# Performance work log

Measured on AMD Instinct MI355X. Metric: run time of the kernel, lower is better.

The kernel has to match this reference:

```python
import jax, jax.numpy as jnp
import numpy as np

D_MODEL = 2048
NUM_HEAD = 16
HEAD_DIM = D_MODEL // NUM_HEAD


def setup_inputs() -> dict:
    key = jax.random.key(0)
    ks = jax.random.split(key, 5)
    scale = 1.0 / np.sqrt(D_MODEL)
    x = jax.random.normal(ks[0], (2, 2048, D_MODEL), dtype=jnp.float32)
    wq = jax.random.normal(ks[1], (D_MODEL, D_MODEL), dtype=jnp.float32) * scale
    wk = jax.random.normal(ks[2], (D_MODEL, D_MODEL), dtype=jnp.float32) * scale
    wv = jax.random.normal(ks[3], (D_MODEL, D_MODEL), dtype=jnp.float32) * scale
    wo = jax.random.normal(ks[4], (D_MODEL, D_MODEL), dtype=jnp.float32) * scale
    return {"x": x, "wq": wq, "wk": wk, "wv": wv, "wo": wo}


def _split_heads(t):
    # [B, T, D] -> [B, H, T, dk]
    B, T, _ = t.shape
    return t.reshape(B, T, NUM_HEAD, HEAD_DIM).transpose(0, 2, 1, 3)


def reference(x, wq, wk, wv, wo):
    # nn.Linear computes x @ W.T; weights here are [out, in]
    Q = _split_heads(x @ wq.T)
    K = _split_heads(x @ wk.T)
    V = _split_heads(x @ wv.T)
    scale = 1.0 / jnp.sqrt(jnp.asarray(HEAD_DIM, dtype=x.dtype))
    score = jnp.einsum('bhqd,bhkd->bhqk', Q, K) * scale
    Tq = score.shape[-2]
    causal_mask = jnp.triu(jnp.ones((Tq, Tq), dtype=bool), k=1)
    score = jnp.where(causal_mask, -jnp.inf, score)
    attn = jax.nn.softmax(score, axis=-1)
    out = jnp.einsum('bhqk,bhkd->bhqd', attn, V)
    B, H, T, dk = out.shape
    out = out.transpose(0, 2, 1, 3).reshape(B, T, H * dk)
    return out @ wo.T
```

## Files before the change

kernel.cpp:

```cpp
#include <hip/hip_runtime.h>

#define DM    2048
#define NH    16
#define HD    128
#define TSEQ  2048
#define BATCH 2
#define MROWS (BATCH * TSEQ)

typedef __bf16 bf16_t;
typedef __bf16 bf16x8 __attribute__((ext_vector_type(8)));
typedef __bf16 bf16x4 __attribute__((ext_vector_type(4)));
typedef float  f32x4  __attribute__((ext_vector_type(4)));
typedef float  f32x16 __attribute__((ext_vector_type(16)));
typedef unsigned short u16x8 __attribute__((ext_vector_type(8)));
typedef unsigned int   u32;

static __device__ __forceinline__ unsigned short f2bf_bits(float f) {
  unsigned u = __builtin_bit_cast(unsigned, f);
  u += 0x7fffu + ((u >> 16) & 1u);
  return (unsigned short)(u >> 16);
}
static __device__ __forceinline__ bf16_t f2bf(float f) {
  unsigned short h = f2bf_bits(f);
  return __builtin_bit_cast(bf16_t, h);
}

static __device__ __forceinline__ void gll16(const void* g, void* lds) {
  __builtin_amdgcn_global_load_lds(
      (const __attribute__((address_space(1))) unsigned int*)g,
      (__attribute__((address_space(3))) unsigned int*)lds, 16, 0, 0);
}

static __device__ __forceinline__ float fast_exp2(float x) {
#if __has_builtin(__builtin_amdgcn_exp2f)
  return __builtin_amdgcn_exp2f(x);
#else
  return exp2f(x);
#endif
}
static __device__ __forceinline__ float fast_rcp(float x) {
#if __has_builtin(__builtin_amdgcn_rcpf)
  return __builtin_amdgcn_rcpf(x);
#else
  return 1.0f / x;
#endif
}

static __device__ __forceinline__ u32 cvtpk(float a, float b) {
  u32 d;
  asm("v_cvt_pk_bf16_f32 %0, %1, %2" : "=v"(d) : "v"(a), "v"(b));
  return d;
}
static __device__ __forceinline__ void pl32swap(u32& a, u32& b) {
  asm volatile("v_permlane32_swap_b32 %0, %1" : "+v"(a), "+v"(b));
}

__global__ void cvt_bf16(const float* __restrict__ s, bf16_t* __restrict__ d, int n8) {
  int i = blockIdx.x * blockDim.x + threadIdx.x;
  if (i >= n8) return;
  const float4* sp = reinterpret_cast<const float4*>(s);
  float4 a = sp[2 * i], b = sp[2 * i + 1];
  u16x8 o;
  o[0] = f2bf_bits(a.x); o[1] = f2bf_bits(a.y); o[2] = f2bf_bits(a.z); o[3] = f2bf_bits(a.w);
  o[4] = f2bf_bits(b.x); o[5] = f2bf_bits(b.y); o[6] = f2bf_bits(b.z); o[7] = f2bf_bits(b.w);
  reinterpret_cast<u16x8*>(d)[i] = o;
}

__global__ void cvt_bf16_w4(const float* __restrict__ s0, const float* __restrict__ s1,
                            const float* __restrict__ s2, const float* __restrict__ s3,
                            bf16_t* __restrict__ d, int n8seg) {
  int i = blockIdx.x * blockDim.x + threadIdx.x;
  if (i >= n8seg) return;
  const int seg = blockIdx.y;
  const float* s = (seg == 0) ? s0 : (seg == 1) ? s1 : (seg == 2) ? s2 : s3;
  const float4* sp = reinterpret_cast<const float4*>(s);
  float4 a = sp[2 * i], b = sp[2 * i + 1];
  u16x8 o;
  o[0] = f2bf_bits(a.x); o[1] = f2bf_bits(a.y); o[2] = f2bf_bits(a.z); o[3] = f2bf_bits(a.w);
  o[4] = f2bf_bits(b.x); o[5] = f2bf_bits(b.y); o[6] = f2bf_bits(b.z); o[7] = f2bf_bits(b.w);
  reinterpret_cast<u16x8*>(d + (size_t)seg * DM * DM)[i] = o;
}

template <int OUTM>
__global__ __launch_bounds__(512, 1) void gemm_3buf(
    const bf16_t* __restrict__ A, const bf16_t* __restrict__ B,
    void* __restrict__ Cq, void* __restrict__ Ck, void* __restrict__ Cv) {
  __shared__ bf16_t Asm[3][256 * 64];
  __shared__ bf16_t Bsm[3][128 * 64];
  const int tid = threadIdx.x;
  const int l = tid & 63, w = tid >> 6;
  const int wm = w >> 1, wn = w & 1;
  const int m0 = blockIdx.y * 256, n0 = blockIdx.x * 128;
  const int NT = DM / 64;

  auto SA = [&](int t, int buf, int s) {
    const int rowbase = s * 64 + w * 8;
    const int row = rowbase + (l >> 3);
    const int ug = (l & 7) ^ (row & 7);
    const int tc = (t < NT) ? t : 0;
    gll16(A + (size_t)(m0 + row) * DM + tc * 64 + ug * 8,
          (char*)Asm[buf] + rowbase * 128);
  };
  auto SB = [&](int t, int buf, int s) {
    const int rowbase = s * 64 + w * 8;
    const int row = rowbase + (l >> 3);
    const int ug = (l & 7) ^ (row & 7);
    const int tc = (t < NT) ? t : 0;
    gll16(B + (size_t)(n0 + row) * DM + tc * 64 + ug * 8,
          (char*)Bsm[buf] + rowbase * 128);
  };

  f32x4 acc[4][4] = {};

#pragma unroll
  for (int s = 0; s < 4; ++s) SA(0, 0, s);
  SB(0, 0, 0); SB(0, 0, 1);
#pragma unroll
  for (int s = 0; s < 4; ++s) SA(1, 1, s);
  SB(1, 1, 0); SB(1, 1, 1);
  asm volatile("s_waitcnt vmcnt(6)" ::: "memory");
  __builtin_amdgcn_s_barrier();
  __builtin_amdgcn_sched_barrier(0);

  for (int j = 0; j < NT; ++j) {
    const int bj = j % 3, bs = (j + 2) % 3;
    const char* Ab_ = (const char*)Asm[bj];
    const char* Bb_ = (const char*)Bsm[bj];
    bf16x8 af[4][2], bfr[4][2];

#pragma unroll
    for (int mi = 0; mi < 4; ++mi)
#pragma unroll
      for (int kh = 0; kh < 2; ++kh) {
        const int row = wm * 64 + mi * 16 + (l & 15);
        const int u = (kh * 4 + (l >> 4)) ^ (row & 7);
        af[mi][kh] = *reinterpret_cast<const bf16x8*>(Ab_ + row * 128 + u * 16);
      }
#pragma unroll
    for (int ni = 0; ni < 4; ++ni)
#pragma unroll
      for (int kh = 0; kh < 2; ++kh) {
        const int row = wn * 64 + ni * 16 + (l & 15);
        const int u = (kh * 4 + (l >> 4)) ^ (row & 7);
        bfr[ni][kh] = *reinterpret_cast<const bf16x8*>(Bb_ + row * 128 + u * 16);
      }

    SA(j + 2, bs, 0); SA(j + 2, bs, 1); SA(j + 2, bs, 2); SA(j + 2, bs, 3);
    SB(j + 2, bs, 0); SB(j + 2, bs, 1);
    __builtin_amdgcn_sched_barrier(0);

    __builtin_amdgcn_s_setprio(1);
#pragma unroll
    for (int kh = 0; kh < 2; ++kh)
#pragma unroll
      for (int mi = 0; mi < 4; ++mi)
#pragma unroll
        for (int ni = 0; ni < 4; ++ni)
          acc[mi][ni] = __builtin_amdgcn_mfma_f32_16x16x32_bf16(
              af[mi][kh], bfr[ni][kh], acc[mi][ni], 0, 0, 0);
    __builtin_amdgcn_s_setprio(0);

    asm volatile("s_waitcnt vmcnt(6)" ::: "memory");
    __builtin_amdgcn_s_barrier();
    __builtin_amdgcn_sched_barrier(0);
  }

  if constexpr (OUTM == 0) {
    const int proj = n0 >> 11;
    const int nc0 = n0 & (DM - 1);
    if (proj < 2) {
      bf16_t* C = (bf16_t*)(proj == 0 ? Cq : Ck);
#pragma unroll
      for (int mi = 0; mi < 4; ++mi) {
        const int row = m0 + wm * 64 + mi * 16 + ((l >> 4) << 2);
#pragma unroll
        for (int ni = 0; ni < 4; ++ni) {
          const int col = nc0 + wn * 64 + ni * 16 + (l & 15);
#pragma unroll
          for (int r = 0; r < 4; ++r)
            C[(size_t)(row + r) * DM + col] = f2bf(acc[mi][ni][r]);
        }
      }
    } else {
      bf16_t* VT = (bf16_t*)Cv;
#pragma unroll
      for (int mi = 0; mi < 4; ++mi) {
        const int row = m0 + wm * 64 + mi * 16 + ((l >> 4) << 2);
        const int bb = row >> 11, tt = row & (TSEQ - 1);
#pragma unroll
        for (int ni = 0; ni < 4; ++ni) {
          const int col = nc0 + wn * 64 + ni * 16 + (l & 15);
          const int hh = col >> 7, dd = col & (HD - 1);
          bf16x4 pk;
#pragma unroll
          for (int r = 0; r < 4; ++r) pk[r] = f2bf(acc[mi][ni][r]);
          *reinterpret_cast<bf16x4*>(VT + (((size_t)bb * NH + hh) * HD + dd) * TSEQ + tt) = pk;
        }
      }
    }
  } else {
    float* C = (float*)Cq;
#pragma unroll
    for (int mi = 0; mi < 4; ++mi) {
      const int row = m0 + wm * 64 + mi * 16 + ((l >> 4) << 2);
#pragma unroll
      for (int ni = 0; ni < 4; ++ni) {
        const int col = n0 + wn * 64 + ni * 16 + (l & 15);
#pragma unroll
        for (int r = 0; r < 4; ++r)
          C[(size_t)(row + r) * DM + col] = acc[mi][ni][r];
      }
    }
  }
}

#define LDS_TOT 75776
__global__ __launch_bounds__(512, 2) void flash_attn(
    const bf16_t* __restrict__ Q, const bf16_t* __restrict__ Kx,
    const bf16_t* __restrict__ VT, bf16_t* __restrict__ O) {
  __shared__ __align__(16) char Lds[LDS_TOT];

  const int tid = threadIdx.x;
  const int l = tid & 63, w = tid >> 6;
  const int hi = l >> 5, ln31 = l & 31;
  const int qw = w >> 1, kw = w & 1;
  const int bh = blockIdx.y;
  const int b = bh >> 4, h = bh & 15;
  const size_t base   = ((size_t)b * TSEQ) * DM + (size_t)h * HD;
  const size_t vtbase = ((size_t)b * NH + h) * HD * (size_t)TSEQ;
  const float cc = 0.12752775f;

  auto run_qtile = [&](int qb) {
    const int wq0 = qb * 128 + qw * 32;
    const int nt = 2 * qb + 2;

    bf16x8 qf[8];
    {
      const bf16_t* qp = Q + base + (size_t)(wq0 + ln31) * DM + hi * 8;
#pragma unroll
      for (int m = 0; m < 8; ++m)
        qf[m] = *reinterpret_cast<const bf16x8*>(qp + m * 16);
    }

    f32x16 acc[4] = {};
    float mrow = -1e30f, lrow = 0.f;

    auto STAGE = [&](int t, int buf) {
#pragma unroll
      for (int c = 0; c < 2; ++c) {
        const int chunk = w * 2 + c;
        const int krow = chunk * 4 + (l >> 4);
        const int u = l & 15;
        const int ug = (u & 8) | ((u ^ krow) & 7);
        gll16(Kx + base + (size_t)(t * 64 + krow) * DM + ug * 8,
              Lds + buf * 16384 + chunk * 1024);
      }
#pragma unroll
      for (int c = 0; c < 2; ++c) {
        const int ci = w * 2 + c;
        const int d = ci * 8 + (l >> 3);
        const int ug = (l & 7) ^ (l >> 3);
        gll16(VT + vtbase + (size_t)d * TSEQ + t * 64 + ug * 8,
              Lds + 32768 + buf * 16384 + ci * 1024);
      }
    };

    STAGE(0, 0);
    __syncthreads();
    int cur = 0;

    for (int t = 0; t < nt; ++t) {
      if (t + 1 < nt) STAGE(t + 1, cur ^ 1);

      const bool active = (t * 64 + kw * 32 <= wq0 + 31);
      if (active) {
        f32x16 s = {};
        const char* Kb_ = Lds + cur * 16384;
        const int kvr = kw * 32 + ln31;
#pragma unroll
        for (int m = 0; m < 8; ++m) {
          const int u = 2 * m + hi;
          const int uswz = (u & 8) | ((u ^ kvr) & 7);
          const bf16x8 kf = *reinterpret_cast<const bf16x8*>(Kb_ + kvr * 256 + uswz * 16);
          s = __builtin_amdgcn_mfma_f32_32x32x16_bf16(kf, qf[m], s, 0, 0, 0);
        }

        float sv[16];
        const int qg = wq0 + ln31;
#pragma unroll
        for (int r = 0; r < 16; ++r) sv[r] = s[r] * cc;
        if (t * 64 + kw * 32 + 31 > wq0) {
#pragma unroll
          for (int r = 0; r < 16; ++r) {
            const int kvg = t * 64 + kw * 32 + (r & 3) + 8 * (r >> 2) + 4 * hi;
            if (kvg > qg) sv[r] = -3.0e38f;
          }
        }

        float mt = sv[0];
#pragma unroll
        for (int r = 1; r < 16; ++r) mt = fmaxf(mt, sv[r]);
        mt = fmaxf(mt, __shfl_xor(mt, 32, 64));

        if (__any(mt > mrow + 8.0f)) {
          const float mn = fmaxf(mrow, mt);
          const float scl = fast_exp2(mrow - mn);
          mrow = mn;
          lrow *= scl;
#pragma unroll
          for (int r = 0; r < 16; ++r) {
            const float sr = __shfl(scl, (r & 3) + 8 * (r >> 2) + 4 * hi, 64);
            acc[0][r] *= sr; acc[1][r] *= sr; acc[2][r] *= sr; acc[3][r] *= sr;
          }
        }

        float rs = 0.f;
#pragma unroll
        for (int r = 0; r < 16; ++r) {
          const float p = fast_exp2(sv[r] - mrow);
          sv[r] = p;
          rs += p;
        }
        rs += __shfl_xor(rs, 32, 64);
        lrow += rs;

        u32 frag[2][4];
#pragma unroll
        for (int f = 0; f < 2; ++f) {
          const float* p = &sv[f * 8];
          u32 a1 = cvtpk(p[0], p[1]);
          u32 b1 = cvtpk(p[4], p[5]);
          pl32swap(a1, b1);
          u32 a2 = cvtpk(p[2], p[3]);
          u32 b2 = cvtpk(p[6], p[7]);
          pl32swap(a2, b2);
          frag[f][0] = a1; frag[f][1] = a2; frag[f][2] = b1; frag[f][3] = b2;
        }

        const char* Vb_ = Lds + 32768 + cur * 16384;
#pragma unroll
        for (int f = 0; f < 2; ++f) {
          const bf16x8 pf = __builtin_bit_cast(bf16x8, *reinterpret_cast<u32(*)[4]>(frag[f]));
#pragma unroll
          for (int n = 0; n < 4; ++n) {
            const int d = n * 32 + ln31;
            const int u = (kw * 2 + f) * 2 + hi;
            const int uswz = u ^ (d & 7);
            const bf16x8 vf = *reinterpret_cast<const bf16x8*>(Vb_ + d * 128 + uswz * 16);
            acc[n] = __builtin_amdgcn_mfma_f32_32x32x16_bf16(pf, vf, acc[n], 0, 0, 0);
          }
        }
      }
      __syncthreads();
      cur ^= 1;
    }

    {
      float* accb = (float*)(Lds + qw * 16384 + kw * 8192);
      const int nb = (kw == 0) ? 2 : 0;
#pragma unroll
      for (int np = 0; np < 2; ++np) {
        float* dst = accb + np * 1024;
#pragma unroll
        for (int r = 0; r < 16; ++r) {
          const int row = (r & 3) + 8 * (r >> 2) + 4 * hi;
          dst[row * 32 + ln31] = acc[nb + np][r];
        }
      }
      float* mlp = (float*)(Lds + 65536 + qw * 1024 + kw * 512);
      if (hi == 0) { mlp[ln31] = mrow; mlp[32 + ln31] = lrow; }
      __syncthreads();

      const float* mlo = (float*)(Lds + 65536 + qw * 1024 + (kw ^ 1) * 512);
      const float mo = mlo[ln31], lo = mlo[32 + ln31];
      const float mm = fmaxf(mrow, mo);
      const float as = fast_exp2(mrow - mm);
      const float ao = fast_exp2(mo - mm);
      const float rln = fast_rcp(lrow * as + lo * ao);
      float* ml2p = (float*)(Lds + 69632 + qw * 1536 + kw * 768);
      if (hi == 0) { ml2p[ln31] = as; ml2p[32 + ln31] = ao; ml2p[64 + ln31] = rln; }
      __syncthreads();

      const float* accoth = (float*)(Lds + qw * 16384 + (kw ^ 1) * 8192);
      const int nf = (kw == 0) ? 0 : 2;
#pragma unroll
      for (int r = 0; r < 16; ++r) {
        const int row = (r & 3) + 8 * (r >> 2) + 4 * hi;
        const float asr = ml2p[row];
        const float aor = ml2p[32 + row];
        const float rlr = ml2p[64 + row];
        const int q = wq0 + row;
        bf16_t* op = O + base + (size_t)q * DM + ln31;
#pragma unroll
        for (int np = 0; np < 2; ++np) {
          const float vo = (acc[nf + np][r] * asr + accoth[np * 1024 + row * 32 + ln31] * aor) * rlr;
          op[(kw * 2 + np) * 32] = f2bf(vo);
        }
      }
      __syncthreads();
    }
  };

  const int i = blockIdx.x;
  run_qtile(i);
  run_qtile((int)(TSEQ / 128) - 1 - i);
}

extern "C" void kernel_launch(void* const* d_in, const int* in_sizes, int n_in,
                              void* d_out, int out_size, void* d_ws, size_t ws_size,
                              hipStream_t stream) {
  (void)in_sizes; (void)n_in; (void)out_size; (void)ws_size;
  const float* x  = (const float*)d_in[0];
  const float* wq = (const float*)d_in[1];
  const float* wk = (const float*)d_in[2];
  const float* wv = (const float*)d_in[3];
  const float* wo = (const float*)d_in[4];
  float* out = (float*)d_out;

  const size_t nx = (size_t)MROWS * DM;
  const size_t nw = (size_t)DM * DM;
  bf16_t* xb  = (bf16_t*)d_ws;
  bf16_t* wqb = xb + nx;
  bf16_t* Qb  = wqb + 4 * nw;
  bf16_t* Kb  = Qb + nx;
  bf16_t* Vtb = Kb + nx;
  bf16_t* Ab  = Vtb + nx;
  bf16_t* wob = wqb + 3 * nw;

  cvt_bf16<<<(int)(nx / 8 / 256), 256, 0, stream>>>(x, xb, (int)(nx / 8));
  cvt_bf16_w4<<<dim3((int)(nw / 8 / 256), 4), 256, 0, stream>>>(
      wq, wk, wv, wo, wqb, (int)(nw / 8));

  gemm_3buf<0><<<dim3(3 * DM / 128, MROWS / 256), 512, 0, stream>>>(
      xb, wqb, Qb, Kb, Vtb);

  flash_attn<<<dim3(TSEQ / 256, BATCH * NH), 512, 0, stream>>>(Qb, Kb, Vtb, Ab);

  gemm_3buf<1><<<dim3(DM / 128, MROWS / 256), 512, 0, stream>>>(
      Ab, wob, out, nullptr, nullptr);
}
```

Measured before the change: 224.1 us.

## Halve GEMM K-tile to 32 and allow two blocks per CU

The projection GEMM now uses a K-step of 32 instead of 64. This halves the triple-buffered LDS footprint, and the launch bounds are raised to allow two 512-thread blocks per CU. The LDS swizzle and load mapping are rewritten for 64-byte rows, and the wait counts are adjusted to match. The aim is more occupancy to hide memory latency, at the cost of twice as many barriers per K and fewer MFMAs between syncs, with tighter register limits.

```diff
diff --git a/kernel.cpp b/kernel.cpp
--- a/kernel.cpp
+++ b/kernel.cpp
@@ -82,43 +82,37 @@
 }
 
 template <int OUTM>
-__global__ __launch_bounds__(512, 1) void gemm_3buf(
+__global__ __launch_bounds__(512, 2) void gemm_3buf(
     const bf16_t* __restrict__ A, const bf16_t* __restrict__ B,
     void* __restrict__ Cq, void* __restrict__ Ck, void* __restrict__ Cv) {
-  __shared__ bf16_t Asm[3][256 * 64];
-  __shared__ bf16_t Bsm[3][128 * 64];
+  __shared__ bf16_t Asm[3][256 * 32];
+  __shared__ bf16_t Bsm[3][128 * 32];
   const int tid = threadIdx.x;
   const int l = tid & 63, w = tid >> 6;
   const int wm = w >> 1, wn = w & 1;
   const int m0 = blockIdx.y * 256, n0 = blockIdx.x * 128;
-  const int NT = DM / 64;
+  const int NT = DM / 32;
 
   auto SA = [&](int t, int buf, int s) {
-    const int rowbase = s * 64 + w * 8;
-    const int row = rowbase + (l >> 3);
-    const int ug = (l & 7) ^ (row & 7);
+    const int row = s * 128 + (tid >> 2);
+    const int ug = (tid & 3) ^ ((row >> 1) & 3);
     const int tc = (t < NT) ? t : 0;
-    gll16(A + (size_t)(m0 + row) * DM + tc * 64 + ug * 8,
-          (char*)Asm[buf] + rowbase * 128);
+    gll16(A + (size_t)(m0 + row) * DM + tc * 32 + ug * 8,
+          (char*)Asm[buf] + s * 8192 + tid * 16);
   };
-  auto SB = [&](int t, int buf, int s) {
-    const int rowbase = s * 64 + w * 8;
-    const int row = rowbase + (l >> 3);
-    const int ug = (l & 7) ^ (row & 7);
+  auto SB = [&](int t, int buf) {
+    const int row = tid >> 2;
+    const int ug = (tid & 3) ^ ((row >> 1) & 3);
     const int tc = (t < NT) ? t : 0;
-    gll16(B + (size_t)(n0 + row) * DM + tc * 64 + ug * 8,
-          (char*)Bsm[buf] + rowbase * 128);
+    gll16(B + (size_t)(n0 + row) * DM + tc * 32 + ug * 8,
+          (char*)Bsm[buf] + tid * 16);
   };
 
   f32x4 acc[4][4] = {};
 
-#pragma unroll
-  for (int s = 0; s < 4; ++s) SA(0, 0, s);
-  SB(0, 0, 0); SB(0, 0, 1);
-#pragma unroll
-  for (int s = 0; s < 4; ++s) SA(1, 1, s);
-  SB(1, 1, 0); SB(1, 1, 1);
-  asm volatile("s_waitcnt vmcnt(6)" ::: "memory");
+  SA(0, 0, 0); SA(0, 0, 1); SB(0, 0);
+  SA(1, 1, 0); SA(1, 1, 1); SB(1, 1);
+  asm volatile("s_waitcnt vmcnt(3)" ::: "memory");
   __builtin_amdgcn_s_barrier();
   __builtin_amdgcn_sched_barrier(0);
 
@@ -126,41 +120,34 @@
     const int bj = j % 3, bs = (j + 2) % 3;
     const char* Ab_ = (const char*)Asm[bj];
     const char* Bb_ = (const char*)Bsm[bj];
-    bf16x8 af[4][2], bfr[4][2];
-
+    bf16x8 af[4], bfr[4];
+
+#pragma unroll
+    for (int mi = 0; mi < 4; ++mi) {
+      const int row = wm * 64 + mi * 16 + (l & 15);
+      const int u = (l >> 4) ^ ((row >> 1) & 3);
+      af[mi] = *reinterpret_cast<const bf16x8*>(Ab_ + row * 64 + u * 16);
+    }
+#pragma unroll
+    for (int ni = 0; ni < 4; ++ni) {
+      const int row = wn * 64 + ni * 16 + (l & 15);
+      const int u = (l >> 4) ^ ((row >> 1) & 3);
+      bfr[ni] = *reinterpret_cast<const bf16x8*>(Bb_ + row * 64 + u * 16);
+    }
+
+    SA(j + 2, bs, 0); SA(j + 2, bs, 1); SB(j + 2, bs);
+    __builtin_amdgcn_sched_barrier(0);
+
+    __builtin_amdgcn_s_setprio(1);
 #pragma unroll
     for (int mi = 0; mi < 4; ++mi)
 #pragma unroll
-      for (int kh = 0; kh < 2; ++kh) {
-        const int row = wm * 64 + mi * 16 + (l & 15);
-        const int u = (kh * 4 + (l >> 4)) ^ (row & 7);
-        af[mi][kh] = *reinterpret_cast<const bf16x8*>(Ab_ + row * 128 + u * 16);
-      }
-#pragma unroll
-    for (int ni = 0; ni < 4; ++ni)
-#pragma unroll
-      for (int kh = 0; kh < 2; ++kh) {
-        const int row = wn * 64 + ni * 16 + (l & 15);
-        const int u = (kh * 4 + (l >> 4)) ^ (row & 7);
-        bfr[ni][kh] = *reinterpret_cast<const bf16x8*>(Bb_ + row * 128 + u * 16);
-      }
-
-    SA(j + 2, bs, 0); SA(j + 2, bs, 1); SA(j + 2, bs, 2); SA(j + 2, bs, 3);
-    SB(j + 2, bs, 0); SB(j + 2, bs, 1);
-    __builtin_amdgcn_sched_barrier(0);
-
-    __builtin_amdgcn_s_setprio(1);
-#pragma unroll
-    for (int kh = 0; kh < 2; ++kh)
-#pragma unroll
-      for (int mi = 0; mi < 4; ++mi)
-#pragma unroll
-        for (int ni = 0; ni < 4; ++ni)
-          acc[mi][ni] = __builtin_amdgcn_mfma_f32_16x16x32_bf16(
-              af[mi][kh], bfr[ni][kh], acc[mi][ni], 0, 0, 0);
+      for (int ni = 0; ni < 4; ++ni)
+        acc[mi][ni] = __builtin_amdgcn_mfma_f32_16x16x32_bf16(
+            af[mi], bfr[ni], acc[mi][ni], 0, 0, 0);
     __builtin_amdgcn_s_setprio(0);
 
-    asm volatile("s_waitcnt vmcnt(6)" ::: "memory");
+    asm volatile("s_waitcnt vmcnt(3)" ::: "memory");
     __builtin_amdgcn_s_barrier();
     __builtin_amdgcn_sched_barrier(0);
   }
```

Measured after the change: 231.7 us. +3.4%, slower.

## Use 4 waves per GEMM block with 128x64 per-wave tiles

Applied to the files above, without the earlier changes.

The GEMM block shrinks from 8 waves to 4 waves while keeping the 256x128 block tile. Each wave now computes 128x64 outputs with 32 accumulators, which raises the MFMA-to-LDS-read ratio. Loads are reorganised to use a 256-thread cooperative layout, and fragment reads are split per k-half so the next stage's loads can be issued after the first half. The cost is higher register pressure and fewer waves per CU available to hide latency.

```diff
diff --git a/kernel.cpp b/kernel.cpp
--- a/kernel.cpp
+++ b/kernel.cpp
@@ -82,7 +82,7 @@
 }
 
 template <int OUTM>
-__global__ __launch_bounds__(512, 1) void gemm_3buf(
+__global__ __launch_bounds__(256, 1) void gemm_3buf(
     const bf16_t* __restrict__ A, const bf16_t* __restrict__ B,
     void* __restrict__ Cq, void* __restrict__ Ck, void* __restrict__ Cv) {
   __shared__ bf16_t Asm[3][256 * 64];
@@ -94,31 +94,31 @@
   const int NT = DM / 64;
 
   auto SA = [&](int t, int buf, int s) {
-    const int rowbase = s * 64 + w * 8;
-    const int row = rowbase + (l >> 3);
-    const int ug = (l & 7) ^ (row & 7);
+    const int row = s * 32 + (tid >> 3);
+    const int ug = (tid & 7) ^ (row & 7);
     const int tc = (t < NT) ? t : 0;
     gll16(A + (size_t)(m0 + row) * DM + tc * 64 + ug * 8,
-          (char*)Asm[buf] + rowbase * 128);
+          (char*)Asm[buf] + s * 4096 + tid * 16);
   };
   auto SB = [&](int t, int buf, int s) {
-    const int rowbase = s * 64 + w * 8;
-    const int row = rowbase + (l >> 3);
-    const int ug = (l & 7) ^ (row & 7);
+    const int row = s * 32 + (tid >> 3);
+    const int ug = (tid & 7) ^ (row & 7);
     const int tc = (t < NT) ? t : 0;
     gll16(B + (size_t)(n0 + row) * DM + tc * 64 + ug * 8,
-          (char*)Bsm[buf] + rowbase * 128);
+          (char*)Bsm[buf] + s * 4096 + tid * 16);
   };
-
-  f32x4 acc[4][4] = {};
-
-#pragma unroll
-  for (int s = 0; s < 4; ++s) SA(0, 0, s);
-  SB(0, 0, 0); SB(0, 0, 1);
-#pragma unroll
-  for (int s = 0; s < 4; ++s) SA(1, 1, s);
-  SB(1, 1, 0); SB(1, 1, 1);
-  asm volatile("s_waitcnt vmcnt(6)" ::: "memory");
+  auto STAGE = [&](int t, int buf) {
+#pragma unroll
+    for (int s = 0; s < 8; ++s) SA(t, buf, s);
+#pragma unroll
+    for (int s = 0; s < 4; ++s) SB(t, buf, s);
+  };
+
+  f32x4 acc[8][4] = {};
+
+  STAGE(0, 0);
+  STAGE(1, 1);
+  asm volatile("s_waitcnt vmcnt(12)" ::: "memory");
   __builtin_amdgcn_s_barrier();
   __builtin_amdgcn_sched_barrier(0);
 
@@ -126,41 +126,37 @@
     const int bj = j % 3, bs = (j + 2) % 3;
     const char* Ab_ = (const char*)Asm[bj];
     const char* Bb_ = (const char*)Bsm[bj];
-    bf16x8 af[4][2], bfr[4][2];
-
-#pragma unroll
-    for (int mi = 0; mi < 4; ++mi)
-#pragma unroll
-      for (int kh = 0; kh < 2; ++kh) {
-        const int row = wm * 64 + mi * 16 + (l & 15);
+
+#pragma unroll
+    for (int kh = 0; kh < 2; ++kh) {
+      bf16x8 af[8], bfr[4];
+#pragma unroll
+      for (int mi = 0; mi < 8; ++mi) {
+        const int row = wm * 128 + mi * 16 + (l & 15);
         const int u = (kh * 4 + (l >> 4)) ^ (row & 7);
-        af[mi][kh] = *reinterpret_cast<const bf16x8*>(Ab_ + row * 128 + u * 16);
-      }
-#pragma unroll
-    for (int ni = 0; ni < 4; ++ni)
-#pragma unroll
-      for (int kh = 0; kh < 2; ++kh) {
+        af[mi] = *reinterpret_cast<const bf16x8*>(Ab_ + row * 128 + u * 16);
+      }
+#pragma unroll
+      for (int ni = 0; ni < 4; ++ni) {
         const int row = wn * 64 + ni * 16 + (l & 15);
         const int u = (kh * 4 + (l >> 4)) ^ (row & 7);
-        bfr[ni][kh] = *reinterpret_cast<const bf16x8*>(Bb_ + row * 128 + u * 16);
-      }
-
-    SA(j + 2, bs, 0); SA(j + 2, bs, 1); SA(j + 2, bs, 2); SA(j + 2, bs, 3);
-    SB(j + 2, bs, 0); SB(j + 2, bs, 1);
-    __builtin_amdgcn_sched_barrier(0);
-
-    __builtin_amdgcn_s_setprio(1);
-#pragma unroll
-    for (int kh = 0; kh < 2; ++kh)
-#pragma unroll
-      for (int mi = 0; mi < 4; ++mi)
+        bfr[ni] = *reinterpret_cast<const bf16x8*>(Bb_ + row * 128 + u * 16);
+      }
+      if (kh == 0) {
+        STAGE(j + 2, bs);
+        __builtin_amdgcn_sched_barrier(0);
+      }
+      __builtin_amdgcn_s_setprio(1);
+#pragma unroll
+      for (int mi = 0; mi < 8; ++mi)
 #pragma unroll
         for (int ni = 0; ni < 4; ++ni)
           acc[mi][ni] = __builtin_amdgcn_mfma_f32_16x16x32_bf16(
-              af[mi][kh], bfr[ni][kh], acc[mi][ni], 0, 0, 0);
-    __builtin_amdgcn_s_setprio(0);
-
-    asm volatile("s_waitcnt vmcnt(6)" ::: "memory");
+              af[mi], bfr[ni], acc[mi][ni], 0, 0, 0);
+      __builtin_amdgcn_s_setprio(0);
+    }
+
+    asm volatile("s_waitcnt vmcnt(12)" ::: "memory");
     __builtin_amdgcn_s_barrier();
     __builtin_amdgcn_sched_barrier(0);
   }
@@ -171,8 +167,8 @@
     if (proj < 2) {
       bf16_t* C = (bf16_t*)(proj == 0 ? Cq : Ck);
 #pragma unroll
-      for (int mi = 0; mi < 4; ++mi) {
-        const int row = m0 + wm * 64 + mi * 16 + ((l >> 4) << 2);
+      for (int mi = 0; mi < 8; ++mi) {
+        const int row = m0 + wm * 128 + mi * 16 + ((l >> 4) << 2);
 #pragma unroll
         for (int ni = 0; ni < 4; ++ni) {
           const int col = nc0 + wn * 64 + ni * 16 + (l & 15);
@@ -184,8 +180,8 @@
     } else {
       bf16_t* VT = (bf16_t*)Cv;
 #pragma unroll
-      for (int mi = 0; mi < 4; ++mi) {
-        const int row = m0 + wm * 64 + mi * 16 + ((l >> 4) << 2);
+      for (int mi = 0; mi < 8; ++mi) {
+        const int row = m0 + wm * 128 + mi * 16 + ((l >> 4) << 2);
         const int bb = row >> 11, tt = row & (TSEQ - 1);
 #pragma unroll
         for (int ni = 0; ni < 4; ++ni) {
@@ -201,8 +197,8 @@
   } else {
     float* C = (float*)Cq;
 #pragma unroll
-    for (int mi = 0; mi < 4; ++mi) {
-      const int row = m0 + wm * 64 + mi * 16 + ((l >> 4) << 2);
+    for (int mi = 0; mi < 8; ++mi) {
+      const int row = m0 + wm * 128 + mi * 16 + ((l >> 4) << 2);
 #pragma unroll
       for (int ni = 0; ni < 4; ++ni) {
         const int col = n0 + wn * 64 + ni * 16 + (l & 15);
@@ -431,11 +427,11 @@
   cvt_bf16_w4<<<dim3((int)(nw / 8 / 256), 4), 256, 0, stream>>>(
       wq, wk, wv, wo, wqb, (int)(nw / 8));
 
-  gemm_3buf<0><<<dim3(3 * DM / 128, MROWS / 256), 512, 0, stream>>>(
+  gemm_3buf<0><<<dim3(3 * DM / 128, MROWS / 256), 256, 0, stream>>>(
       xb, wqb, Qb, Kb, Vtb);
 
   flash_attn<<<dim3(TSEQ / 256, BATCH * NH), 512, 0, stream>>>(Qb, Kb, Vtb, Ab);
 
-  gemm_3buf<1><<<dim3(DM / 128, MROWS / 256), 512, 0, stream>>>(
+  gemm_3buf<1><<<dim3(DM / 128, MROWS / 256), 256, 0, stream>>>(
       Ab, wob, out, nullptr, nullptr);
 }
```

Measured after the change: 286.1 us. 1.28x slower.
